# Kernel optimization log

Measured on AMD Instinct MI355X. Metric: run time of the kernel, lower is better.

The kernel has to match this reference:

```python
import jax, jax.numpy as jnp
import numpy as np
from jax import lax


def causal_dwconv(x, w, b):
    # x: (b, l, d); w: (k, 1, d) in WIO layout with feature_group_count=d; b: (d,)
    k = w.shape[0]
    y = lax.conv_general_dilated(
        x, w,
        window_strides=(1,),
        padding=[(k - 1, 0)],  # left pad only => causal, equals torch pad=k-1 then slice [:l]
        dimension_numbers=("NWC", "WIO", "NWC"),
        feature_group_count=x.shape[-1],
    )
    return y + b


def setup_inputs() -> dict:
    key = jax.random.key(0)
    ks = jax.random.split(key, 7)
    b, l, d = 4, 4096, 1024
    k1, k2 = 3, 128
    s1 = 1.0 / np.sqrt(k1)  # torch Conv1d init bound ~ 1/sqrt(in_ch/groups * k)
    s2 = 1.0 / np.sqrt(k2)
    sp = 1.0 / np.sqrt(d)
    return {
        "u": jax.random.normal(ks[0], (b, l, d), dtype=jnp.float32),
        "w1": jax.random.normal(ks[1], (k1, 1, d), dtype=jnp.float32) * s1,
        "b1": jax.random.normal(ks[2], (d,), dtype=jnp.float32) * s1,
        "w2": jax.random.normal(ks[3], (k2, 1, d), dtype=jnp.float32) * s2,
        "b2": jax.random.normal(ks[4], (d,), dtype=jnp.float32) * s2,
        "Wp": jax.random.normal(ks[5], (d, d), dtype=jnp.float32) * sp,
        "bp": jax.random.normal(ks[6], (d,), dtype=jnp.float32) * sp,
    }


def reference(u, w1, b1, w2, b2, Wp, bp):
    # conv1 -> silu -> conv2
    h = jax.nn.silu(causal_dwconv(u, w1, b1))
    u_conv2 = causal_dwconv(h, w2, b2)
    # linear projection (torch Linear: u @ Wp.T + bp) -> silu
    u_proj = jax.nn.silu(jnp.einsum("bld,ed->ble", u, Wp) + bp)
    y = u_conv2.astype(jnp.float32) * u_proj.astype(jnp.float32)
    return y.astype(u.dtype)
```

## Files before the change

### kernel.cpp

```cpp
#include <hip/hip_runtime.h>
#include <cstdint>
#include <cstddef>

#define D     1024
#define LSEQ  4096
#define BATCH 4
#define MROWS (BATCH * LSEQ)

typedef __attribute__((ext_vector_type(8))) __bf16 bf16x8;
typedef __attribute__((ext_vector_type(4))) float  f32x4;

__device__ __forceinline__ ushort f2bf(float f) {
  union { float f; uint32_t u; } v; v.f = f;
  uint32_t u = v.u;
  return (ushort)((u + 0x7fffu + ((u >> 16) & 1u)) >> 16);
}

__device__ __forceinline__ float silu_f(float x) { return x / (1.f + expf(-x)); }

__global__ __launch_bounds__(256) void cvt_wp(const float* __restrict__ s,
                                              ushort* __restrict__ d) {
  const int i = (blockIdx.x * 256 + threadIdx.x) * 4;
  const float4 v = *reinterpret_cast<const float4*>(&s[i]);
  ushort4 o;
  o.x = f2bf(v.x); o.y = f2bf(v.y); o.z = f2bf(v.z); o.w = f2bf(v.w);
  *reinterpret_cast<ushort4*>(&d[i]) = o;
}

#define TL1 64
__global__ __launch_bounds__(256) void conv1_silu_cvt(
    const float* __restrict__ u, const float* __restrict__ w1,
    const float* __restrict__ b1, float* __restrict__ h,
    ushort* __restrict__ ubf) {
  const int c  = blockIdx.x * 256 + threadIdx.x;
  const int b  = blockIdx.z;
  const int l0 = blockIdx.y * TL1;
  const size_t base = ((size_t)b * LSEQ) * D + c;
  const float wa = w1[c], wb = w1[D + c], wcc = w1[2 * D + c];
  const float bias = b1[c];
  float x0 = (l0 >= 2) ? u[base + (size_t)(l0 - 2) * D] : 0.f;
  float x1 = (l0 >= 1) ? u[base + (size_t)(l0 - 1) * D] : 0.f;
  #pragma unroll 4
  for (int l = l0; l < l0 + TL1; ++l) {
    const float x2 = u[base + (size_t)l * D];
    const float v = fmaf(x0, wa, fmaf(x1, wb, fmaf(x2, wcc, bias)));
    h[base + (size_t)l * D]   = silu_f(v);
    ubf[base + (size_t)l * D] = f2bf(x2);
    x0 = x1; x1 = x2;
  }
}

#define BM 128
#define BN 128
#define BK 32
__global__ __launch_bounds__(256) void gemm_bias_silu(
    const ushort* __restrict__ A, const ushort* __restrict__ B,
    const float* __restrict__ bp, float* __restrict__ out) {
  __shared__ ushort lsA[BM][BK];
  __shared__ ushort lsB[BN][BK];
  const int tid  = threadIdx.x;
  const int wave = tid >> 6, lane = tid & 63;
  const int m0 = blockIdx.x * BM;
  const int n0 = blockIdx.y * BN;
  const int wr = (wave >> 1) * 64;
  const int wc = (wave & 1) * 64;
  const int fr = lane & 15;
  const int fk = (lane >> 4) * 8;
  const int row0 = tid >> 2,         col0 = (tid & 3) * 8;
  const int row1 = (tid + 256) >> 2, col1 = col0;

  f32x4 acc[4][4];
  #pragma unroll
  for (int i = 0; i < 4; ++i)
    #pragma unroll
    for (int j = 0; j < 4; ++j) acc[i][j] = f32x4{0.f, 0.f, 0.f, 0.f};

  for (int k0 = 0; k0 < D; k0 += BK) {
    *reinterpret_cast<int4*>(&lsA[row0][col0]) =
        *reinterpret_cast<const int4*>(&A[(size_t)(m0 + row0) * D + k0 + col0]);
    *reinterpret_cast<int4*>(&lsA[row1][col1]) =
        *reinterpret_cast<const int4*>(&A[(size_t)(m0 + row1) * D + k0 + col1]);
    *reinterpret_cast<int4*>(&lsB[row0][col0]) =
        *reinterpret_cast<const int4*>(&B[(size_t)(n0 + row0) * D + k0 + col0]);
    *reinterpret_cast<int4*>(&lsB[row1][col1]) =
        *reinterpret_cast<const int4*>(&B[(size_t)(n0 + row1) * D + k0 + col1]);
    __syncthreads();
    bf16x8 af[4], bfr[4];
    #pragma unroll
    for (int i = 0; i < 4; ++i)
      af[i] = *reinterpret_cast<const bf16x8*>(&lsA[wr + i * 16 + fr][fk]);
    #pragma unroll
    for (int j = 0; j < 4; ++j)
      bfr[j] = *reinterpret_cast<const bf16x8*>(&lsB[wc + j * 16 + fr][fk]);
    #pragma unroll
    for (int i = 0; i < 4; ++i)
      #pragma unroll
      for (int j = 0; j < 4; ++j)
        acc[i][j] = __builtin_amdgcn_mfma_f32_16x16x32_bf16(af[i], bfr[j],
                                                            acc[i][j], 0, 0, 0);
    __syncthreads();
  }
  const int ccol  = lane & 15;
  const int rbase = (lane >> 4) * 4;
  #pragma unroll
  for (int i = 0; i < 4; ++i) {
    #pragma unroll
    for (int j = 0; j < 4; ++j) {
      const int gn  = n0 + wc + j * 16 + ccol;
      const float bv = bp[gn];
      #pragma unroll
      for (int r = 0; r < 4; ++r) {
        const int gm = m0 + wr + i * 16 + rbase + r;
        out[(size_t)gm * D + gn] = silu_f(acc[i][j][r] + bv);
      }
    }
  }
}

#define TL4 64
#define RL  16
__global__ __launch_bounds__(256) void conv2_mul(
    const float* __restrict__ h, const float* __restrict__ w2,
    const float* __restrict__ b2, float* __restrict__ out) {
  const int c  = blockIdx.x * 256 + threadIdx.x;
  const int b  = blockIdx.z;
  const int L0 = blockIdx.y * TL4;
  const float* hb  = h   + ((size_t)b * LSEQ) * D + c;
  float*       ob  = out + ((size_t)b * LSEQ) * D + c;
  const float* w2c = w2 + c;
  const float bias = b2[c];

  for (int g = 0; g < TL4 / RL; ++g) {
    const int L = L0 + g * RL;
    float acc[RL];
    #pragma unroll
    for (int r = 0; r < RL; ++r) acc[r] = 0.f;

    float hh[31];
    int jb = L - 127;
    #pragma unroll
    for (int q = 0; q < 31; ++q) {
      const int j = jb + q;
      hh[q] = (j >= 0) ? hb[(size_t)j * D] : 0.f;
    }
    #pragma unroll
    for (int tb = 0; tb < 8; ++tb) {
      #pragma unroll
      for (int i = 0; i < 16; ++i) {
        const float wv = w2c[(size_t)(tb * 16 + i) * D];
        #pragma unroll
        for (int r = 0; r < RL; ++r)
          acc[r] = fmaf(wv, hh[i + r], acc[r]);
      }
      if (tb < 7) {
        jb += 16;
        #pragma unroll
        for (int q = 0; q < 15; ++q) hh[q] = hh[q + 16];
        #pragma unroll
        for (int q = 15; q < 31; ++q) {
          const int j = jb + q;
          hh[q] = (j >= 0) ? hb[(size_t)j * D] : 0.f;
        }
      }
    }
    #pragma unroll
    for (int r = 0; r < RL; ++r) {
      const size_t p = (size_t)(L + r);
      const float pj = ob[p * D];
      ob[p * D] = (acc[r] + bias) * pj;
    }
  }
}

extern "C" void kernel_launch(void* const* d_in, const int* in_sizes, int n_in,
                              void* d_out, int out_size, void* d_ws,
                              size_t ws_size, hipStream_t stream) {
  const float* u  = (const float*)d_in[0];
  const float* w1 = (const float*)d_in[1];
  const float* b1 = (const float*)d_in[2];
  const float* w2 = (const float*)d_in[3];
  const float* b2 = (const float*)d_in[4];
  const float* Wp = (const float*)d_in[5];
  const float* bp = (const float*)d_in[6];
  float* out = (float*)d_out;

  char* ws = (char*)d_ws;
  float*  h    = (float*)(ws);
  ushort* ubf  = (ushort*)(ws + (size_t)67108864);
  ushort* wpbf = (ushort*)(ws + (size_t)100663296);

  cvt_wp<<<dim3(D * D / 1024), 256, 0, stream>>>(Wp, wpbf);
  conv1_silu_cvt<<<dim3(D / 256, LSEQ / TL1, BATCH), 256, 0, stream>>>(
      u, w1, b1, h, ubf);
  gemm_bias_silu<<<dim3(MROWS / BM, D / BN), 256, 0, stream>>>(
      ubf, wpbf, bp, out);
  conv2_mul<<<dim3(D / 256, LSEQ / TL4, BATCH), 256, 0, stream>>>(
      h, w2, b2, out);
}
```

Measured before the change: 330.2 us.

## Store conv1 output as bf16, stage conv2 halo in LDS, use direct global-to-LDS loads

The conv1 intermediate is now written in bf16, which halves its write and read traffic. conv2 is reorganised so each block stages a 255-row by 64-channel tile, including the 127-row causal halo, in shared memory once and then reads the sliding window from LDS rather than re-reading global memory. The GEMM loads its A and B tiles with global_load_lds builtins that write straight to LDS and skip the register round trip. Rounding the conv1 activations to bf16 adds a precision loss before the 128-tap convolution.

```diff
diff --git a/kernel.cpp b/kernel.cpp
--- a/kernel.cpp
+++ b/kernel.cpp
@@ -15,8 +15,16 @@
   uint32_t u = v.u;
   return (ushort)((u + 0x7fffu + ((u >> 16) & 1u)) >> 16);
 }
-
+__device__ __forceinline__ float bf2f(ushort h) {
+  union { uint32_t u; float f; } v; v.u = ((uint32_t)h) << 16; return v.f;
+}
 __device__ __forceinline__ float silu_f(float x) { return x / (1.f + expf(-x)); }
+
+__device__ __forceinline__ void gl_lds16(const void* g, void* l) {
+  __builtin_amdgcn_global_load_lds(
+      (const __attribute__((address_space(1))) void*)g,
+      (__attribute__((address_space(3))) void*)l, 16, 0, 0);
+}
 
 __global__ __launch_bounds__(256) void cvt_wp(const float* __restrict__ s,
                                               ushort* __restrict__ d) {
@@ -30,7 +38,7 @@
 #define TL1 64
 __global__ __launch_bounds__(256) void conv1_silu_cvt(
     const float* __restrict__ u, const float* __restrict__ w1,
-    const float* __restrict__ b1, float* __restrict__ h,
+    const float* __restrict__ b1, ushort* __restrict__ h,
     ushort* __restrict__ ubf) {
   const int c  = blockIdx.x * 256 + threadIdx.x;
   const int b  = blockIdx.z;
@@ -44,7 +52,7 @@
   for (int l = l0; l < l0 + TL1; ++l) {
     const float x2 = u[base + (size_t)l * D];
     const float v = fmaf(x0, wa, fmaf(x1, wb, fmaf(x2, wcc, bias)));
-    h[base + (size_t)l * D]   = silu_f(v);
+    h[base + (size_t)l * D]   = f2bf(silu_f(v));
     ubf[base + (size_t)l * D] = f2bf(x2);
     x0 = x1; x1 = x2;
   }
@@ -56,8 +64,8 @@
 __global__ __launch_bounds__(256) void gemm_bias_silu(
     const ushort* __restrict__ A, const ushort* __restrict__ B,
     const float* __restrict__ bp, float* __restrict__ out) {
-  __shared__ ushort lsA[BM][BK];
-  __shared__ ushort lsB[BN][BK];
+  __shared__ __align__(16) ushort lsA[BM][BK];
+  __shared__ __align__(16) ushort lsB[BN][BK];
   const int tid  = threadIdx.x;
   const int wave = tid >> 6, lane = tid & 63;
   const int m0 = blockIdx.x * BM;
@@ -66,8 +74,12 @@
   const int wc = (wave & 1) * 64;
   const int fr = lane & 15;
   const int fk = (lane >> 4) * 8;
-  const int row0 = tid >> 2,         col0 = (tid & 3) * 8;
-  const int row1 = (tid + 256) >> 2, col1 = col0;
+  const int o0 = (wave * 2 + 0) * 1024 + lane * 16;
+  const int o1 = (wave * 2 + 1) * 1024 + lane * 16;
+  const int r0 = o0 >> 6, c0e = (o0 & 63) >> 1;
+  const int r1 = o1 >> 6, c1e = (o1 & 63) >> 1;
+  char* ldsA = (char*)&lsA[0][0];
+  char* ldsB = (char*)&lsB[0][0];
 
   f32x4 acc[4][4];
   #pragma unroll
@@ -76,14 +88,10 @@
     for (int j = 0; j < 4; ++j) acc[i][j] = f32x4{0.f, 0.f, 0.f, 0.f};
 
   for (int k0 = 0; k0 < D; k0 += BK) {
-    *reinterpret_cast<int4*>(&lsA[row0][col0]) =
-        *reinterpret_cast<const int4*>(&A[(size_t)(m0 + row0) * D + k0 + col0]);
-    *reinterpret_cast<int4*>(&lsA[row1][col1]) =
-        *reinterpret_cast<const int4*>(&A[(size_t)(m0 + row1) * D + k0 + col1]);
-    *reinterpret_cast<int4*>(&lsB[row0][col0]) =
-        *reinterpret_cast<const int4*>(&B[(size_t)(n0 + row0) * D + k0 + col0]);
-    *reinterpret_cast<int4*>(&lsB[row1][col1]) =
-        *reinterpret_cast<const int4*>(&B[(size_t)(n0 + row1) * D + k0 + col1]);
+    gl_lds16(&A[(size_t)(m0 + r0) * D + k0 + c0e], ldsA + o0);
+    gl_lds16(&A[(size_t)(m0 + r1) * D + k0 + c1e], ldsA + o1);
+    gl_lds16(&B[(size_t)(n0 + r0) * D + k0 + c0e], ldsB + o0);
+    gl_lds16(&B[(size_t)(n0 + r1) * D + k0 + c1e], ldsB + o1);
     __syncthreads();
     bf16x8 af[4], bfr[4];
     #pragma unroll
@@ -117,39 +125,62 @@
   }
 }
 
-#define TL4 64
-#define RL  16
+#define C2CH   64
+#define C2TL   128
+#define C2ROWS (C2TL + 127)
+#define C2PADB 136
 __global__ __launch_bounds__(256) void conv2_mul(
-    const float* __restrict__ h, const float* __restrict__ w2,
+    const ushort* __restrict__ h, const float* __restrict__ w2,
     const float* __restrict__ b2, float* __restrict__ out) {
-  const int c  = blockIdx.x * 256 + threadIdx.x;
-  const int b  = blockIdx.z;
-  const int L0 = blockIdx.y * TL4;
-  const float* hb  = h   + ((size_t)b * LSEQ) * D + c;
-  float*       ob  = out + ((size_t)b * LSEQ) * D + c;
-  const float* w2c = w2 + c;
-  const float bias = b2[c];
-
-  for (int g = 0; g < TL4 / RL; ++g) {
-    const int L = L0 + g * RL;
-    float acc[RL];
-    #pragma unroll
-    for (int r = 0; r < RL; ++r) acc[r] = 0.f;
+  __shared__ __align__(16) char hsb[C2ROWS * C2PADB];
+  const int tid = threadIdx.x;
+  const int c0  = blockIdx.x * C2CH;
+  const int L0  = blockIdx.y * C2TL;
+  const int b   = blockIdx.z;
+  const ushort* hb = h + ((size_t)b * LSEQ) * D;
+
+  const int sr = tid >> 4;
+  const int sc = (tid & 15) * 4;
+  #pragma unroll
+  for (int pass = 0; pass < 16; ++pass) {
+    const int r = pass * 16 + sr;
+    if (r < C2ROWS) {
+      const int g = L0 - 127 + r;
+      unsigned long long v = 0ull;
+      if (g >= 0)
+        v = *reinterpret_cast<const unsigned long long*>(
+                &hb[(size_t)g * D + c0 + sc]);
+      *reinterpret_cast<unsigned long long*>(&hsb[r * C2PADB + sc * 2]) = v;
+    }
+  }
+  __syncthreads();
+
+  const int c  = tid & 63;
+  const int lq = tid >> 6;
+  const float bias = b2[c0 + c];
+  const float* w2c = w2 + c0 + c;
+  float* ob = out + ((size_t)b * LSEQ) * D + c0 + c;
+
+  #pragma unroll
+  for (int g2 = 0; g2 < 2; ++g2) {
+    const int ls0 = lq * 32 + g2 * 16;
+    float acc[16];
+    #pragma unroll
+    for (int r = 0; r < 16; ++r) acc[r] = 0.f;
 
     float hh[31];
-    int jb = L - 127;
-    #pragma unroll
-    for (int q = 0; q < 31; ++q) {
-      const int j = jb + q;
-      hh[q] = (j >= 0) ? hb[(size_t)j * D] : 0.f;
-    }
+    int jb = ls0;
+    #pragma unroll
+    for (int q = 0; q < 31; ++q)
+      hh[q] = bf2f(*reinterpret_cast<const ushort*>(
+                   &hsb[(jb + q) * C2PADB + c * 2]));
     #pragma unroll
     for (int tb = 0; tb < 8; ++tb) {
       #pragma unroll
       for (int i = 0; i < 16; ++i) {
         const float wv = w2c[(size_t)(tb * 16 + i) * D];
         #pragma unroll
-        for (int r = 0; r < RL; ++r)
+        for (int r = 0; r < 16; ++r)
           acc[r] = fmaf(wv, hh[i + r], acc[r]);
       }
       if (tb < 7) {
@@ -157,17 +188,16 @@
         #pragma unroll
         for (int q = 0; q < 15; ++q) hh[q] = hh[q + 16];
         #pragma unroll
-        for (int q = 15; q < 31; ++q) {
-          const int j = jb + q;
-          hh[q] = (j >= 0) ? hb[(size_t)j * D] : 0.f;
-        }
+        for (int q = 15; q < 31; ++q)
+          hh[q] = bf2f(*reinterpret_cast<const ushort*>(
+                       &hsb[(jb + q) * C2PADB + c * 2]));
       }
     }
     #pragma unroll
-    for (int r = 0; r < RL; ++r) {
-      const size_t p = (size_t)(L + r);
-      const float pj = ob[p * D];
-      ob[p * D] = (acc[r] + bias) * pj;
+    for (int r = 0; r < 16; ++r) {
+      const size_t p = (size_t)(L0 + ls0 + r) * D;
+      const float pj = ob[p];
+      ob[p] = (acc[r] + bias) * pj;
     }
   }
 }
@@ -185,15 +215,15 @@
   float* out = (float*)d_out;
 
   char* ws = (char*)d_ws;
-  float*  h    = (float*)(ws);
-  ushort* ubf  = (ushort*)(ws + (size_t)67108864);
-  ushort* wpbf = (ushort*)(ws + (size_t)100663296);
+  ushort* h    = (ushort*)(ws);
+  ushort* ubf  = (ushort*)(ws + (size_t)33554432);
+  ushort* wpbf = (ushort*)(ws + (size_t)67108864);
 
   cvt_wp<<<dim3(D * D / 1024), 256, 0, stream>>>(Wp, wpbf);
   conv1_silu_cvt<<<dim3(D / 256, LSEQ / TL1, BATCH), 256, 0, stream>>>(
       u, w1, b1, h, ubf);
   gemm_bias_silu<<<dim3(MROWS / BM, D / BN), 256, 0, stream>>>(
       ubf, wpbf, bp, out);
-  conv2_mul<<<dim3(D / 256, LSEQ / TL4, BATCH), 256, 0, stream>>>(
+  conv2_mul<<<dim3(D / C2CH, LSEQ / C2TL, BATCH), 256, 0, stream>>>(
       h, w2, b2, out);
 }
```

Result: slower. 507.0 us (+53.6%).
